# Performance work log

Hardware: AMD Instinct MI355X
Metric: run time of the kernel (lower is better)

## Reference

```python
import jax, jax.numpy as jnp
import numpy as np

B, S, D, H, L, F, V = 8, 4096, 1024, 16, 6, 2048, 256
DH = D // H

def _pe(seq, dim):
    pos = jnp.arange(seq, dtype=jnp.float32)[:, None]
    div = jnp.exp(jnp.arange(0, dim, 2, dtype=jnp.float32) * (-np.log(10000.0) / dim))
    pe = jnp.zeros((seq, dim), jnp.float32)
    pe = pe.at[:, 0::2].set(jnp.sin(pos * div))
    pe = pe.at[:, 1::2].set(jnp.cos(pos * div))
    return pe

def _ln(x, w, b):
    m = x.mean(-1, keepdims=True)
    v = ((x - m) ** 2).mean(-1, keepdims=True)
    return (x - m) * jax.lax.rsqrt(v + 1e-5) * w + b

def setup_inputs():
    key = jax.random.key(0)
    ks = jax.random.split(key, 8)
    s = 0.02
    return {
        'tgt': jax.random.normal(ks[0], (B, S, D), jnp.float32),
        'in_proj_w': jax.random.normal(ks[1], (L, 3 * D, D), jnp.float32) * s,
        'in_proj_b': jnp.zeros((L, 3 * D), jnp.float32),
        'out_proj_w': jax.random.normal(ks[2], (L, D, D), jnp.float32) * s,
        'out_proj_b': jnp.zeros((L, D), jnp.float32),
        'ln1_w': jnp.ones((L, D), jnp.float32), 'ln1_b': jnp.zeros((L, D), jnp.float32),
        'lin1_w': jax.random.normal(ks[3], (L, F, D), jnp.float32) * s,
        'lin1_b': jnp.zeros((L, F), jnp.float32),
        'lin2_w': jax.random.normal(ks[4], (L, D, F), jnp.float32) * s,
        'lin2_b': jnp.zeros((L, D), jnp.float32),
        'ln2_w': jnp.ones((L, D), jnp.float32), 'ln2_b': jnp.zeros((L, D), jnp.float32),
        'w_out': jax.random.normal(ks[5], (V, D), jnp.float32) * s,
        'b_out': jnp.zeros((V,), jnp.float32),
    }

def reference(tgt, in_proj_w, in_proj_b, out_proj_w, out_proj_b, ln1_w, ln1_b,
              lin1_w, lin1_b, lin2_w, lin2_b, ln2_w, ln2_b, w_out, b_out):
    # eval-mode cached decode step of CachedDecoderOnly.forward (dropout inactive)
    out = tgt + _pe(S, D)[None]  # [B,S,D]
    for i in range(L):
        q = out[:, -1:, :]  # query is only the last token
        wq, wk, wv = jnp.split(in_proj_w[i], 3, axis=0)
        bq, bk, bv = jnp.split(in_proj_b[i], 3)
        Q = (q @ wq.T + bq).reshape(B, 1, H, DH)
        K = (out @ wk.T + bk).reshape(B, -1, H, DH)
        Vv = (out @ wv.T + bv).reshape(B, -1, H, DH)
        sc = jnp.einsum('bqhd,bkhd->bhqk', Q, K) / jnp.sqrt(jnp.float32(DH))
        a = jax.nn.softmax(sc, axis=-1)
        o = jnp.einsum('bhqk,bkhd->bqhd', a, Vv).reshape(B, 1, D)
        o = o @ out_proj_w[i].T + out_proj_b[i]
        y = _ln(q + o, ln1_w[i], ln1_b[i])
        ff = jax.nn.relu(y @ lin1_w[i].T + lin1_b[i]) @ lin2_w[i].T + lin2_b[i]
        out = _ln(y + ff, ln2_w[i], ln2_b[i])  # [B,1,D] -> src for next layer
    return out @ w_out.T + b_out  # [B,1,V]
```

## Files before the change

kernel.cpp:

```cpp
#include <hip/hip_runtime.h>
#include <hip/hip_bf16.h>

#define BB 8
#define SS 4096
#define DD 1024
#define HH 16
#define LL 6
#define FF 2048
#define VV 256
#define NC 64

typedef __attribute__((ext_vector_type(8))) short bf16x8;
typedef __attribute__((ext_vector_type(4))) float f32x4;

__device__ __forceinline__ unsigned short f2bf(float f) {
    union { float f; unsigned u; } v; v.f = f;
    unsigned r = v.u + 0x7FFFu + ((v.u >> 16) & 1u);
    return (unsigned short)(r >> 16);
}

__global__ __launch_bounds__(256) void pelast_kernel(float* __restrict__ pl) {
    for (int i = threadIdx.x; i < DD / 2; i += 256) {
        float div = expf((-logf(10000.0f) / (float)DD) * (float)(2 * i));
        float a = (float)(SS - 1) * div;
        pl[2 * i]     = sinf(a);
        pl[2 * i + 1] = cosf(a);
    }
}

__global__ __launch_bounds__(256) void xprep_kernel(const float* __restrict__ tgt,
                                                    unsigned* __restrict__ xb)
{
    int s0 = blockIdx.x * 8, b = blockIdx.y;
    for (int i = threadIdx.x; i < DD / 2; i += 256) {
        float div = expf((-logf(10000.0f) / (float)DD) * (float)(2 * i));
        float a0 = (float)s0 * div;
        float sa = sinf(a0), ca = cosf(a0);
        float sd = sinf(div), cd = cosf(div);
        #pragma unroll
        for (int r = 0; r < 8; ++r) {
            float2 t = reinterpret_cast<const float2*>(tgt + ((long)b * SS + s0 + r) * DD)[i];
            unsigned lo = f2bf(t.x + sa), hi = f2bf(t.y + ca);
            xb[((long)b * SS + s0 + r) * (DD / 2) + i] = lo | (hi << 16);
            float sn = sa * cd + ca * sd;
            ca = ca * cd - sa * sd;
            sa = sn;
        }
    }
}

template <int K, int RELU, int MODE>
__global__ __launch_bounds__(256) void gemm8k(
    const float* __restrict__ A, long sA,
    const float* __restrict__ A2, long sA2,
    const float* __restrict__ W,
    const float* __restrict__ bias,
    const float* __restrict__ R1, long sR1,
    const float* __restrict__ R2, long sR2,
    const float* __restrict__ lnw, const float* __restrict__ lnb,
    const float* __restrict__ lnsrc,
    float* __restrict__ C, int N)
{
    int wave = threadIdx.x >> 6, lane = threadIdx.x & 63;
    int n = blockIdx.x * 4 + wave;
    if (n >= N) return;

    float mean[8], rstd[8];
    if (MODE != 0) {
        const float* S = (MODE == 1) ? A : lnsrc;
        long ss = (MODE == 1) ? sA : 1024L;
        const int SK = (MODE == 1) ? K : 1024;
        #pragma unroll
        for (int m = 0; m < 8; ++m) {
            float s1 = 0.f, s2 = 0.f;
            const float4* Sr = reinterpret_cast<const float4*>(S + (long)m * ss);
            #pragma unroll
            for (int k4 = 0; k4 < SK / 256; ++k4) {
                float4 a = Sr[k4 * 64 + lane];
                s1 += a.x + a.y + a.z + a.w;
                s2 += a.x * a.x + a.y * a.y + a.z * a.z + a.w * a.w;
            }
            for (int off = 32; off; off >>= 1) {
                s1 += __shfl_xor(s1, off, 64);
                s2 += __shfl_xor(s2, off, 64);
            }
            float mu = s1 / (float)SK;
            mean[m] = mu;
            rstd[m] = rsqrtf(s2 / (float)SK - mu * mu + 1e-5f);
        }
    }

    float acc[8] = {0.f,0.f,0.f,0.f,0.f,0.f,0.f,0.f};
    const float4* W4 = reinterpret_cast<const float4*>(W + (long)n * K);
    float4 wv[K / 256];
    #pragma unroll
    for (int kb = 0; kb < K / 256; ++kb) wv[kb] = W4[kb * 64 + lane];
    #pragma unroll
    for (int kb = 0; kb < K / 256; ++kb) {
        int k4 = kb * 64 + lane;
        float4 w = wv[kb];
        float4 lw, lb;
        if (MODE == 1) {
            lw = reinterpret_cast<const float4*>(lnw)[k4];
            lb = reinterpret_cast<const float4*>(lnb)[k4];
        }
        #pragma unroll
        for (int m = 0; m < 8; ++m) {
            float4 a = reinterpret_cast<const float4*>(A + (long)m * sA)[k4];
            if (A2) {
                float4 a2 = reinterpret_cast<const float4*>(A2 + (long)m * sA2)[k4];
                a.x += a2.x; a.y += a2.y; a.z += a2.z; a.w += a2.w;
            }
            if (MODE == 1) {
                float mu = mean[m], rs = rstd[m];
                a.x = (a.x - mu) * rs * lw.x + lb.x;
                a.y = (a.y - mu) * rs * lw.y + lb.y;
                a.z = (a.z - mu) * rs * lw.z + lb.z;
                a.w = (a.w - mu) * rs * lw.w + lb.w;
            }
            acc[m] += a.x * w.x + a.y * w.y + a.z * w.z + a.w * w.w;
        }
    }
    #pragma unroll
    for (int m = 0; m < 8; ++m)
        for (int off = 32; off; off >>= 1) acc[m] += __shfl_xor(acc[m], off, 64);
    if (lane == 0) {
        float bs = bias ? bias[n] : 0.f;
        #pragma unroll
        for (int m = 0; m < 8; ++m) {
            float v = acc[m] + bs;
            if (MODE == 0) {
                if (R1) v += R1[(long)m * sR1 + n];
                if (R2) v += R2[(long)m * sR2 + n];
            }
            if (MODE == 2)
                v += (lnsrc[(long)m * 1024 + n] - mean[m]) * rstd[m] * lnw[n] + lnb[n];
            if (RELU) v = fmaxf(v, 0.f);
            C[(long)m * N + n] = v;
        }
    }
}

__global__ __launch_bounds__(256) void u_kernel(const float* __restrict__ Q,
                                                const float* __restrict__ wk,
                                                unsigned short* __restrict__ ub)
{
    int h = blockIdx.y;
    int e = blockIdx.x * 256 + threadIdx.x;
    __shared__ float qs[8][64];
    for (int idx = threadIdx.x; idx < 512; idx += 256) {
        int b = idx >> 6, d = idx & 63;
        qs[b][d] = Q[(long)b * DD + h * 64 + d];
    }
    __syncthreads();
    float acc[8] = {0.f,0.f,0.f,0.f,0.f,0.f,0.f,0.f};
    for (int d = 0; d < 64; ++d) {
        float wv = wk[(long)(h * 64 + d) * DD + e];
        #pragma unroll
        for (int b = 0; b < 8; ++b) acc[b] += qs[b][d] * wv;
    }
    #pragma unroll
    for (int b = 0; b < 8; ++b)
        ub[((long)(b * HH + h)) * DD + e] = f2bf(acc[b]);
}

__global__ __launch_bounds__(512, 4) void attn_kernel(
    const unsigned short* __restrict__ xb,
    const unsigned short* __restrict__ ub,
    float* __restrict__ ctxp, float* __restrict__ ml)
{
    int sc = blockIdx.x, b = blockIdx.y;
    int wave = threadIdx.x >> 6, lane = threadIdx.x & 63;
    int q = lane >> 4, n = lane & 15;
    __shared__ float scs[2][16][66];
    __shared__ unsigned short P[16 * 64];

    int s0 = sc * 64;

    {
        int st = wave >> 1, kh = wave & 1;
        int s = s0 + st * 16 + n;
        const unsigned short* xrow = xb + ((long)b * SS + s) * DD + kh * 512;
        const unsigned short* urow = ub + ((long)(b * HH) + n) * DD + kh * 512;
        f32x4 acc = {0.f, 0.f, 0.f, 0.f};
        #pragma unroll
        for (int ks = 0; ks < 16; ++ks) {
            int e0 = ks * 32 + q * 8;
            bf16x8 a  = *reinterpret_cast<const bf16x8*>(urow + e0);
            bf16x8 xv = *reinterpret_cast<const bf16x8*>(xrow + e0);
            acc = __builtin_amdgcn_mfma_f32_16x16x32_bf16(a, xv, acc, 0, 0, 0);
        }
        #pragma unroll
        for (int r = 0; r < 4; ++r) scs[kh][q * 4 + r][st * 16 + n] = acc[r];
    }
    __syncthreads();

    {
        int h = threadIdx.x >> 5, l = threadIdx.x & 31;
        float2 v0 = *reinterpret_cast<const float2*>(&scs[0][h][l * 2]);
        float2 v1 = *reinterpret_cast<const float2*>(&scs[1][h][l * 2]);
        float a0 = (v0.x + v1.x) * 0.125f;
        float a1 = (v0.y + v1.y) * 0.125f;
        float mx = fmaxf(a0, a1);
        #pragma unroll
        for (int off = 16; off; off >>= 1) mx = fmaxf(mx, __shfl_xor(mx, off, 32));
        float e0 = expf(a0 - mx), e1 = expf(a1 - mx);
        float sum = e0 + e1;
        #pragma unroll
        for (int off = 16; off; off >>= 1) sum += __shfl_xor(sum, off, 32);
        unsigned d0 = (unsigned)f2bf(e0) | ((unsigned)f2bf(e1) << 16);
        char* Pb = reinterpret_cast<char*>(P);
        *reinterpret_cast<unsigned*>(Pb + ((h * 128 + l * 4) ^ ((h & 7) << 4))) = d0;
        if (l == 0) {
            long mi = ((long)sc * BB + b) * HH + h;
            ml[mi * 2] = mx;
            ml[mi * 2 + 1] = sum;
        }
    }
    __syncthreads();

    {
        const char* Pb = reinterpret_cast<const char*>(P);
        bf16x8 pa[2];
        #pragma unroll
        for (int ks2 = 0; ks2 < 2; ++ks2) {
            int sb = ks2 * 32 + q * 8;
            pa[ks2] = *reinterpret_cast<const bf16x8*>(
                Pb + ((n * 128 + sb * 2) ^ ((n & 7) << 4)));
        }
        f32x4 cacc[8];
        #pragma unroll
        for (int t = 0; t < 8; ++t) cacc[t] = (f32x4){0.f, 0.f, 0.f, 0.f};
        #pragma unroll
        for (int ks2 = 0; ks2 < 2; ++ks2) {
            int sb = ks2 * 32 + q * 8;
            const unsigned short* xbase = xb + ((long)b * SS + s0 + sb) * DD;
            #pragma unroll
            for (int t = 0; t < 8; ++t) {
                int e = wave * 128 + t * 16 + n;
                union { unsigned short sh[8]; bf16x8 v; } bu;
                #pragma unroll
                for (int j = 0; j < 8; ++j)
                    bu.sh[j] = xbase[(long)j * DD + e];
                cacc[t] = __builtin_amdgcn_mfma_f32_16x16x32_bf16(pa[ks2], bu.v, cacc[t], 0, 0, 0);
            }
        }
        long base = (((long)sc * BB + b) * HH) * DD;
        #pragma unroll
        for (int t = 0; t < 8; ++t) {
            int e = wave * 128 + t * 16 + n;
            #pragma unroll
            for (int r = 0; r < 4; ++r)
                ctxp[base + (long)(q * 4 + r) * DD + e] = cacc[t][r];
        }
    }
}

__global__ __launch_bounds__(256) void ctxred_kernel(const float* __restrict__ ctxp,
                                                     const float* __restrict__ ml,
                                                     float* __restrict__ ctx)
{
    int row = blockIdx.x;
    __shared__ float scl[NC];
    int t = threadIdx.x;
    if (t < 64) {
        float m = ml[((long)t * BB * HH + row) * 2];
        float l = ml[((long)t * BB * HH + row) * 2 + 1];
        float M = m;
        #pragma unroll
        for (int off = 32; off; off >>= 1) M = fmaxf(M, __shfl_xor(M, off, 64));
        float e = expf(m - M);
        float L = e * l;
        #pragma unroll
        for (int off = 32; off; off >>= 1) L += __shfl_xor(L, off, 64);
        scl[t] = e / L;
    }
    __syncthreads();
    int e = blockIdx.y * 256 + t;
    float s = 0.f;
    #pragma unroll 8
    for (int c = 0; c < NC; ++c)
        s += scl[c] * ctxp[((long)c * BB * HH + row) * DD + e];
    ctx[(long)row * DD + e] = s;
}

__global__ __launch_bounds__(256) void ov_kernel(const float* __restrict__ ctx,
                                                 const float* __restrict__ wv,
                                                 const float* __restrict__ bv,
                                                 float* __restrict__ o)
{
    int wave = threadIdx.x >> 6, lane = threadIdx.x & 63;
    int j = blockIdx.x * 4 + wave;
    if (j >= DD) return;
    int h = j >> 6;
    float acc[8] = {0.f,0.f,0.f,0.f,0.f,0.f,0.f,0.f};
    const float4* w4 = reinterpret_cast<const float4*>(wv + (long)j * DD);
    float4 wreg[4];
    #pragma unroll
    for (int kb = 0; kb < 4; ++kb) wreg[kb] = w4[kb * 64 + lane];
    #pragma unroll
    for (int kb = 0; kb < 4; ++kb) {
        int k4 = kb * 64 + lane;
        float4 w = wreg[kb];
        #pragma unroll
        for (int b = 0; b < 8; ++b) {
            float4 a = reinterpret_cast<const float4*>(ctx + ((long)(b * HH + h)) * DD)[k4];
            acc[b] += a.x * w.x + a.y * w.y + a.z * w.z + a.w * w.w;
        }
    }
    #pragma unroll
    for (int b = 0; b < 8; ++b)
        for (int off = 32; off; off >>= 1) acc[b] += __shfl_xor(acc[b], off, 64);
    if (lane == 0) {
        float bs = bv[j];
        #pragma unroll
        for (int b = 0; b < 8; ++b) o[(long)b * DD + j] = acc[b] + bs;
    }
}

extern "C" void kernel_launch(void* const* d_in, const int* in_sizes, int n_in,
                              void* d_out, int out_size, void* d_ws, size_t ws_size,
                              hipStream_t stream)
{
    const float* tgt        = (const float*)d_in[0];
    const float* in_proj_w  = (const float*)d_in[1];
    const float* in_proj_b  = (const float*)d_in[2];
    const float* out_proj_w = (const float*)d_in[3];
    const float* out_proj_b = (const float*)d_in[4];
    const float* ln1_w      = (const float*)d_in[5];
    const float* ln1_b      = (const float*)d_in[6];
    const float* lin1_w     = (const float*)d_in[7];
    const float* lin1_b     = (const float*)d_in[8];
    const float* lin2_w     = (const float*)d_in[9];
    const float* lin2_b     = (const float*)d_in[10];
    const float* ln2_w      = (const float*)d_in[11];
    const float* ln2_b      = (const float*)d_in[12];
    const float* w_out      = (const float*)d_in[13];
    const float* b_out      = (const float*)d_in[14];

    float* ws = (float*)d_ws;
    long off = 0;
    unsigned short* xb = (unsigned short*)(ws + off); off += (long)BB * SS * DD / 2;
    float* ctxp = ws + off;  off += (long)NC * BB * HH * DD;
    float* ml   = ws + off;  off += (long)NC * BB * HH * 2;
    float* ctx  = ws + off;  off += (long)BB * HH * DD;
    unsigned short* ub = (unsigned short*)(ws + off); off += (long)BB * HH * DD / 2;
    float* pl   = ws + off;  off += DD;
    float* Q    = ws + off;  off += (long)BB * DD;
    float* o    = ws + off;  off += (long)BB * DD;
    float* vb   = ws + off;  off += (long)BB * DD;
    float* o2   = ws + off;  off += (long)BB * DD;
    float* hb   = ws + off;  off += (long)BB * FF;
    float* z    = ws + off;  off += (long)BB * DD;

    const float* tgt_last = tgt + (long)(SS - 1) * DD;

    pelast_kernel<<<1, 256, 0, stream>>>(pl);
    xprep_kernel<<<dim3(SS / 8, BB), 256, 0, stream>>>(tgt, (unsigned*)xb);

    gemm8k<1024, 0, 0><<<DD / 4, 256, 0, stream>>>(
        tgt_last, (long)SS * DD, pl, 0L, in_proj_w, in_proj_b,
        nullptr, 0L, nullptr, 0L, nullptr, nullptr, nullptr, Q, DD);

    u_kernel<<<dim3(4, 16), 256, 0, stream>>>(Q, in_proj_w + (long)DD * DD, ub);

    attn_kernel<<<dim3(NC, BB), 512, 0, stream>>>(xb, ub, ctxp, ml);
    ctxred_kernel<<<dim3(BB * HH, 4), 256, 0, stream>>>(ctxp, ml, ctx);

    ov_kernel<<<DD / 4, 256, 0, stream>>>(ctx, in_proj_w + 2L * DD * DD, in_proj_b + 2 * DD, o);

    gemm8k<1024, 0, 0><<<DD / 4, 256, 0, stream>>>(
        o, (long)DD, nullptr, 0L, out_proj_w, out_proj_b,
        tgt_last, (long)SS * DD, pl, 0L, nullptr, nullptr, nullptr, o2, DD);
    gemm8k<1024, 1, 1><<<FF / 4, 256, 0, stream>>>(
        o2, (long)DD, nullptr, 0L, lin1_w, lin1_b,
        nullptr, 0L, nullptr, 0L, ln1_w, ln1_b, nullptr, hb, FF);
    gemm8k<2048, 0, 2><<<DD / 4, 256, 0, stream>>>(
        hb, (long)FF, nullptr, 0L, lin2_w, lin2_b,
        nullptr, 0L, nullptr, 0L, ln1_w, ln1_b, o2, z, DD);

    for (int i = 1; i < LL; ++i) {
        const float* wv_i  = in_proj_w + (long)i * 3 * DD * DD + 2L * DD * DD;
        const float* bv_i  = in_proj_b + (long)i * 3 * DD + 2 * DD;
        const float* l2w_p = ln2_w + (long)(i - 1) * DD;
        const float* l2b_p = ln2_b + (long)(i - 1) * DD;
        const float* l1w   = ln1_w + (long)i * DD;
        const float* l1b   = ln1_b + (long)i * DD;
        gemm8k<1024, 0, 1><<<DD / 4, 256, 0, stream>>>(
            z, (long)DD, nullptr, 0L, wv_i, bv_i,
            nullptr, 0L, nullptr, 0L, l2w_p, l2b_p, nullptr, vb, DD);
        gemm8k<1024, 0, 2><<<DD / 4, 256, 0, stream>>>(
            vb, (long)DD, nullptr, 0L,
            out_proj_w + (long)i * DD * DD, out_proj_b + (long)i * DD,
            nullptr, 0L, nullptr, 0L, l2w_p, l2b_p, z, o2, DD);
        gemm8k<1024, 1, 1><<<FF / 4, 256, 0, stream>>>(
            o2, (long)DD, nullptr, 0L,
            lin1_w + (long)i * FF * DD, lin1_b + (long)i * FF,
            nullptr, 0L, nullptr, 0L, l1w, l1b, nullptr, hb, FF);
        gemm8k<2048, 0, 2><<<DD / 4, 256, 0, stream>>>(
            hb, (long)FF, nullptr, 0L,
            lin2_w + (long)i * DD * FF, lin2_b + (long)i * DD,
            nullptr, 0L, nullptr, 0L, l1w, l1b, o2, z, DD);
    }

    gemm8k<1024, 0, 1><<<VV / 4, 256, 0, stream>>>(
        z, (long)DD, nullptr, 0L, w_out, b_out,
        nullptr, 0L, nullptr, 0L,
        ln2_w + (long)(LL - 1) * DD, ln2_b + (long)(LL - 1) * DD, nullptr,
        (float*)d_out, VV);
}
```

Before: 611.5 us.

## Fuse post-attention GEMV chain into one persistent kernel with grid barriers

The roughly 25 small GEMV launches after attention (ov, out_proj, FFN for every layer, and the final projection) become a single persistent kernel of 256 blocks. Stages are separated by an atomic-counter grid barrier, and each wave loops over output rows. This removes per-launch overhead and the tail gaps between dependent kernels. The cost is that it relies on all 256 blocks being resident at once, and each barrier adds spin-wait and fence latency.

New measurement: 1.648 ms. 2.7x slower.

```diff
diff --git a/kernel.cpp b/kernel.cpp
--- a/kernel.cpp
+++ b/kernel.cpp
@@ -9,6 +9,7 @@
 #define FF 2048
 #define VV 256
 #define NC 64
+#define TB 256
 
 typedef __attribute__((ext_vector_type(8))) short bf16x8;
 typedef __attribute__((ext_vector_type(4))) float f32x4;
@@ -19,7 +20,27 @@
     return (unsigned short)(r >> 16);
 }
 
-__global__ __launch_bounds__(256) void pelast_kernel(float* __restrict__ pl) {
+__device__ __forceinline__ void gbar(unsigned* bar) {
+    __syncthreads();
+    if (threadIdx.x == 0) {
+        __threadfence();
+        unsigned g = __hip_atomic_load(&bar[1], __ATOMIC_ACQUIRE, __HIP_MEMORY_SCOPE_AGENT);
+        unsigned a = __hip_atomic_fetch_add(&bar[0], 1u, __ATOMIC_ACQ_REL, __HIP_MEMORY_SCOPE_AGENT);
+        if (a == TB - 1) {
+            __hip_atomic_store(&bar[0], 0u, __ATOMIC_RELAXED, __HIP_MEMORY_SCOPE_AGENT);
+            __hip_atomic_store(&bar[1], g + 1u, __ATOMIC_RELEASE, __HIP_MEMORY_SCOPE_AGENT);
+        } else {
+            while (__hip_atomic_load(&bar[1], __ATOMIC_ACQUIRE, __HIP_MEMORY_SCOPE_AGENT) == g)
+                __builtin_amdgcn_s_sleep(8);
+        }
+        __threadfence();
+    }
+    __syncthreads();
+}
+
+__global__ __launch_bounds__(256) void pelast_kernel(float* __restrict__ pl,
+                                                     unsigned* __restrict__ bar) {
+    if (threadIdx.x == 0) { bar[0] = 0u; bar[1] = 0u; }
     for (int i = threadIdx.x; i < DD / 2; i += 256) {
         float div = expf((-logf(10000.0f) / (float)DD) * (float)(2 * i));
         float a = (float)(SS - 1) * div;
@@ -284,38 +305,193 @@
     ctx[(long)row * DD + e] = s;
 }
 
-__global__ __launch_bounds__(256) void ov_kernel(const float* __restrict__ ctx,
-                                                 const float* __restrict__ wv,
-                                                 const float* __restrict__ bv,
-                                                 float* __restrict__ o)
-{
-    int wave = threadIdx.x >> 6, lane = threadIdx.x & 63;
-    int j = blockIdx.x * 4 + wave;
-    if (j >= DD) return;
-    int h = j >> 6;
-    float acc[8] = {0.f,0.f,0.f,0.f,0.f,0.f,0.f,0.f};
-    const float4* w4 = reinterpret_cast<const float4*>(wv + (long)j * DD);
-    float4 wreg[4];
-    #pragma unroll
-    for (int kb = 0; kb < 4; ++kb) wreg[kb] = w4[kb * 64 + lane];
-    #pragma unroll
-    for (int kb = 0; kb < 4; ++kb) {
-        int k4 = kb * 64 + lane;
-        float4 w = wreg[kb];
-        #pragma unroll
-        for (int b = 0; b < 8; ++b) {
-            float4 a = reinterpret_cast<const float4*>(ctx + ((long)(b * HH + h)) * DD)[k4];
-            acc[b] += a.x * w.x + a.y * w.y + a.z * w.z + a.w * w.w;
-        }
-    }
-    #pragma unroll
-    for (int b = 0; b < 8; ++b)
-        for (int off = 32; off; off >>= 1) acc[b] += __shfl_xor(acc[b], off, 64);
-    if (lane == 0) {
-        float bs = bv[j];
-        #pragma unroll
-        for (int b = 0; b < 8; ++b) o[(long)b * DD + j] = acc[b] + bs;
-    }
+
+__device__ __forceinline__ void ov_stage(int gw, int lane,
+    const float* __restrict__ ctx, const float* __restrict__ wv,
+    const float* __restrict__ bv, float* __restrict__ o)
+{
+    for (int j = gw; j < DD; j += 1024) {
+        int h = j >> 6;
+        float acc[8] = {0.f,0.f,0.f,0.f,0.f,0.f,0.f,0.f};
+        const float4* w4 = reinterpret_cast<const float4*>(wv + (long)j * DD);
+        float4 wreg[4];
+        #pragma unroll
+        for (int kb = 0; kb < 4; ++kb) wreg[kb] = w4[kb * 64 + lane];
+        #pragma unroll
+        for (int kb = 0; kb < 4; ++kb) {
+            int k4 = kb * 64 + lane;
+            float4 w = wreg[kb];
+            #pragma unroll
+            for (int b = 0; b < 8; ++b) {
+                float4 a = reinterpret_cast<const float4*>(ctx + ((long)(b * HH + h)) * DD)[k4];
+                acc[b] += a.x * w.x + a.y * w.y + a.z * w.z + a.w * w.w;
+            }
+        }
+        #pragma unroll
+        for (int b = 0; b < 8; ++b)
+            for (int off = 32; off; off >>= 1) acc[b] += __shfl_xor(acc[b], off, 64);
+        if (lane == 0) {
+            float bs = bv[j];
+            #pragma unroll
+            for (int b = 0; b < 8; ++b) o[(long)b * DD + j] = acc[b] + bs;
+        }
+    }
+}
+
+template <int K, int RELU, int MODE>
+__device__ __forceinline__ void gemv_stage(int gw, int lane,
+    const float* __restrict__ A, long sA,
+    const float* __restrict__ A2, long sA2,
+    const float* __restrict__ W,
+    const float* __restrict__ bias,
+    const float* __restrict__ R1, long sR1,
+    const float* __restrict__ R2, long sR2,
+    const float* __restrict__ lnw, const float* __restrict__ lnb,
+    const float* __restrict__ lnsrc,
+    float* __restrict__ C, int N)
+{
+    float mean[8], rstd[8];
+    if (MODE != 0) {
+        const float* S = (MODE == 1) ? A : lnsrc;
+        long ss = (MODE == 1) ? sA : 1024L;
+        const int SK = (MODE == 1) ? K : 1024;
+        #pragma unroll
+        for (int m = 0; m < 8; ++m) {
+            float s1 = 0.f, s2 = 0.f;
+            const float4* Sr = reinterpret_cast<const float4*>(S + (long)m * ss);
+            #pragma unroll
+            for (int k4 = 0; k4 < SK / 256; ++k4) {
+                float4 a = Sr[k4 * 64 + lane];
+                s1 += a.x + a.y + a.z + a.w;
+                s2 += a.x * a.x + a.y * a.y + a.z * a.z + a.w * a.w;
+            }
+            for (int off = 32; off; off >>= 1) {
+                s1 += __shfl_xor(s1, off, 64);
+                s2 += __shfl_xor(s2, off, 64);
+            }
+            float mu = s1 / (float)SK;
+            mean[m] = mu;
+            rstd[m] = rsqrtf(s2 / (float)SK - mu * mu + 1e-5f);
+        }
+    }
+
+    for (int n = gw; n < N; n += 1024) {
+        float acc[8] = {0.f,0.f,0.f,0.f,0.f,0.f,0.f,0.f};
+        const float4* W4 = reinterpret_cast<const float4*>(W + (long)n * K);
+        float4 wv[K / 256];
+        #pragma unroll
+        for (int kb = 0; kb < K / 256; ++kb) wv[kb] = W4[kb * 64 + lane];
+        #pragma unroll
+        for (int kb = 0; kb < K / 256; ++kb) {
+            int k4 = kb * 64 + lane;
+            float4 w = wv[kb];
+            float4 lw, lb;
+            if (MODE == 1) {
+                lw = reinterpret_cast<const float4*>(lnw)[k4];
+                lb = reinterpret_cast<const float4*>(lnb)[k4];
+            }
+            #pragma unroll
+            for (int m = 0; m < 8; ++m) {
+                float4 a = reinterpret_cast<const float4*>(A + (long)m * sA)[k4];
+                if (A2) {
+                    float4 a2 = reinterpret_cast<const float4*>(A2 + (long)m * sA2)[k4];
+                    a.x += a2.x; a.y += a2.y; a.z += a2.z; a.w += a2.w;
+                }
+                if (MODE == 1) {
+                    float mu = mean[m], rs = rstd[m];
+                    a.x = (a.x - mu) * rs * lw.x + lb.x;
+                    a.y = (a.y - mu) * rs * lw.y + lb.y;
+                    a.z = (a.z - mu) * rs * lw.z + lb.z;
+                    a.w = (a.w - mu) * rs * lw.w + lb.w;
+                }
+                acc[m] += a.x * w.x + a.y * w.y + a.z * w.z + a.w * w.w;
+            }
+        }
+        #pragma unroll
+        for (int m = 0; m < 8; ++m)
+            for (int off = 32; off; off >>= 1) acc[m] += __shfl_xor(acc[m], off, 64);
+        if (lane == 0) {
+            float bs = bias ? bias[n] : 0.f;
+            #pragma unroll
+            for (int m = 0; m < 8; ++m) {
+                float v = acc[m] + bs;
+                if (MODE == 0) {
+                    if (R1) v += R1[(long)m * sR1 + n];
+                    if (R2) v += R2[(long)m * sR2 + n];
+                }
+                if (MODE == 2)
+                    v += (lnsrc[(long)m * 1024 + n] - mean[m]) * rstd[m] * lnw[n] + lnb[n];
+                if (RELU) v = fmaxf(v, 0.f);
+                C[(long)m * N + n] = v;
+            }
+        }
+    }
+}
+
+__global__ __launch_bounds__(256) void tail_kernel(
+    const float* ctx, const float* in_proj_w, const float* in_proj_b,
+    const float* tgt_last, const float* pl,
+    const float* out_proj_w, const float* out_proj_b,
+    const float* ln1_w, const float* ln1_b,
+    const float* lin1_w, const float* lin1_b,
+    const float* lin2_w, const float* lin2_b,
+    const float* ln2_w, const float* ln2_b,
+    const float* w_out, const float* b_out,
+    float* o, float* o2, float* hb, float* z, float* vb, float* dout,
+    unsigned* bar)
+{
+    int gw   = (blockIdx.x << 2) + (threadIdx.x >> 6);
+    int lane = threadIdx.x & 63;
+
+    ov_stage(gw, lane, ctx, in_proj_w + 2L * DD * DD, in_proj_b + 2 * DD, o);
+    gbar(bar);
+
+    gemv_stage<1024, 0, 0>(gw, lane, o, (long)DD, nullptr, 0L,
+                           out_proj_w, out_proj_b,
+                           tgt_last, (long)SS * DD, pl, 0L,
+                           nullptr, nullptr, nullptr, o2, DD);
+    gbar(bar);
+    gemv_stage<1024, 1, 1>(gw, lane, o2, (long)DD, nullptr, 0L,
+                           lin1_w, lin1_b, nullptr, 0L, nullptr, 0L,
+                           ln1_w, ln1_b, nullptr, hb, FF);
+    gbar(bar);
+    gemv_stage<2048, 0, 2>(gw, lane, hb, (long)FF, nullptr, 0L,
+                           lin2_w, lin2_b, nullptr, 0L, nullptr, 0L,
+                           ln1_w, ln1_b, o2, z, DD);
+
+    for (int i = 1; i < LL; ++i) {
+        const float* wv_i  = in_proj_w + (long)i * 3 * DD * DD + 2L * DD * DD;
+        const float* bv_i  = in_proj_b + (long)i * 3 * DD + 2 * DD;
+        const float* l2w_p = ln2_w + (long)(i - 1) * DD;
+        const float* l2b_p = ln2_b + (long)(i - 1) * DD;
+        const float* l1w   = ln1_w + (long)i * DD;
+        const float* l1b   = ln1_b + (long)i * DD;
+        gbar(bar);
+        gemv_stage<1024, 0, 1>(gw, lane, z, (long)DD, nullptr, 0L,
+                               wv_i, bv_i, nullptr, 0L, nullptr, 0L,
+                               l2w_p, l2b_p, nullptr, vb, DD);
+        gbar(bar);
+        gemv_stage<1024, 0, 2>(gw, lane, vb, (long)DD, nullptr, 0L,
+                               out_proj_w + (long)i * DD * DD, out_proj_b + (long)i * DD,
+                               nullptr, 0L, nullptr, 0L,
+                               l2w_p, l2b_p, z, o2, DD);
+        gbar(bar);
+        gemv_stage<1024, 1, 1>(gw, lane, o2, (long)DD, nullptr, 0L,
+                               lin1_w + (long)i * FF * DD, lin1_b + (long)i * FF,
+                               nullptr, 0L, nullptr, 0L,
+                               l1w, l1b, nullptr, hb, FF);
+        gbar(bar);
+        gemv_stage<2048, 0, 2>(gw, lane, hb, (long)FF, nullptr, 0L,
+                               lin2_w + (long)i * DD * FF, lin2_b + (long)i * DD,
+                               nullptr, 0L, nullptr, 0L,
+                               l1w, l1b, o2, z, DD);
+    }
+    gbar(bar);
+
+    gemv_stage<1024, 0, 1>(gw, lane, z, (long)DD, nullptr, 0L,
+                           w_out, b_out, nullptr, 0L, nullptr, 0L,
+                           ln2_w + (long)(LL - 1) * DD, ln2_b + (long)(LL - 1) * DD,
+                           nullptr, dout, VV);
 }
 
 extern "C" void kernel_launch(void* const* d_in, const int* in_sizes, int n_in,
@@ -352,10 +528,12 @@
     float* o2   = ws + off;  off += (long)BB * DD;
     float* hb   = ws + off;  off += (long)BB * FF;
     float* z    = ws + off;  off += (long)BB * DD;
+    unsigned* bar = (unsigned*)(ws + off); off += 16;
 
     const float* tgt_last = tgt + (long)(SS - 1) * DD;
-
-    pelast_kernel<<<1, 256, 0, stream>>>(pl);
+    float* dout = (float*)d_out;
+
+    pelast_kernel<<<1, 256, 0, stream>>>(pl, bar);
     xprep_kernel<<<dim3(SS / 8, BB), 256, 0, stream>>>(tgt, (unsigned*)xb);
 
     gemm8k<1024, 0, 0><<<DD / 4, 256, 0, stream>>>(
@@ -367,45 +545,9 @@
     attn_kernel<<<dim3(NC, BB), 512, 0, stream>>>(xb, ub, ctxp, ml);
     ctxred_kernel<<<dim3(BB * HH, 4), 256, 0, stream>>>(ctxp, ml, ctx);
 
-    ov_kernel<<<DD / 4, 256, 0, stream>>>(ctx, in_proj_w + 2L * DD * DD, in_proj_b + 2 * DD, o);
-
-    gemm8k<1024, 0, 0><<<DD / 4, 256, 0, stream>>>(
-        o, (long)DD, nullptr, 0L, out_proj_w, out_proj_b,
-        tgt_last, (long)SS * DD, pl, 0L, nullptr, nullptr, nullptr, o2, DD);
-    gemm8k<1024, 1, 1><<<FF / 4, 256, 0, stream>>>(
-        o2, (long)DD, nullptr, 0L, lin1_w, lin1_b,
-        nullptr, 0L, nullptr, 0L, ln1_w, ln1_b, nullptr, hb, FF);
-    gemm8k<2048, 0, 2><<<DD / 4, 256, 0, stream>>>(
-        hb, (long)FF, nullptr, 0L, lin2_w, lin2_b,
-        nullptr, 0L, nullptr, 0L, ln1_w, ln1_b, o2, z, DD);
-
-    for (int i = 1; i < LL; ++i) {
-        const float* wv_i  = in_proj_w + (long)i * 3 * DD * DD + 2L * DD * DD;
-        const float* bv_i  = in_proj_b + (long)i * 3 * DD + 2 * DD;
-        const float* l2w_p = ln2_w + (long)(i - 1) * DD;
-        const float* l2b_p = ln2_b + (long)(i - 1) * DD;
-        const float* l1w   = ln1_w + (long)i * DD;
-        const float* l1b   = ln1_b + (long)i * DD;
-        gemm8k<1024, 0, 1><<<DD / 4, 256, 0, stream>>>(
-            z, (long)DD, nullptr, 0L, wv_i, bv_i,
-            nullptr, 0L, nullptr, 0L, l2w_p, l2b_p, nullptr, vb, DD);
-        gemm8k<1024, 0, 2><<<DD / 4, 256, 0, stream>>>(
-            vb, (long)DD, nullptr, 0L,
-            out_proj_w + (long)i * DD * DD, out_proj_b + (long)i * DD,
-            nullptr, 0L, nullptr, 0L, l2w_p, l2b_p, z, o2, DD);
-        gemm8k<1024, 1, 1><<<FF / 4, 256, 0, stream>>>(
-            o2, (long)DD, nullptr, 0L,
-            lin1_w + (long)i * FF * DD, lin1_b + (long)i * FF,
-            nullptr, 0L, nullptr, 0L, l1w, l1b, nullptr, hb, FF);
-        gemm8k<2048, 0, 2><<<DD / 4, 256, 0, stream>>>(
-            hb, (long)FF, nullptr, 0L,
-            lin2_w + (long)i * DD * FF, lin2_b + (long)i * DD,
-            nullptr, 0L, nullptr, 0L, l1w, l1b, o2, z, DD);
-    }
-
-    gemm8k<1024, 0, 1><<<VV / 4, 256, 0, stream>>>(
-        z, (long)DD, nullptr, 0L, w_out, b_out,
-        nullptr, 0L, nullptr, 0L,
-        ln2_w + (long)(LL - 1) * DD, ln2_b + (long)(LL - 1) * DD, nullptr,
-        (float*)d_out, VV);
-}
+    tail_kernel<<<TB, 256, 0, stream>>>(
+        ctx, in_proj_w, in_proj_b, tgt_last, pl,
+        out_proj_w, out_proj_b, ln1_w, ln1_b,
+        lin1_w, lin1_b, lin2_w, lin2_b, ln2_w, ln2_b,
+        w_out, b_out, o, o2, hb, z, vb, dout, bar);
+}
```
